# Kernel optimization log

Measured on AMD Instinct MI355X. Metric: run time of the kernel, lower is better.

The kernel has to match this reference:

```python
import jax, jax.numpy as jnp
import numpy as np

NUM_FEATURES = 8
HIDDEN = 64
IN_DIM = NUM_FEATURES + 6  # 14


def _lstm_cell(x, h, c, W_ih, W_hh, b_ih, b_hh):
    # torch gate order: i, f, g, o
    gates = x @ W_ih.T + h @ W_hh.T + b_ih + b_hh
    i, f, g, o = jnp.split(gates, 4, axis=-1)
    c_new = jax.nn.sigmoid(f) * c + jax.nn.sigmoid(i) * jnp.tanh(g)
    h_new = jax.nn.sigmoid(o) * jnp.tanh(c_new)
    return h_new, c_new


def setup_inputs() -> dict:
    key = jax.random.key(0)
    ks = jax.random.split(key, 20)
    T = 20000
    s = 0.05
    inp = {
        "encoder_out": jax.random.normal(ks[0], (1024, 64), jnp.float32),
        "h0": jax.random.normal(ks[1], (2, HIDDEN), jnp.float32),
        "c0": jax.random.normal(ks[2], (2, HIDDEN), jnp.float32),
        "difficulty": jax.random.normal(ks[3], (6,), jnp.float32),
        "target": jax.random.normal(ks[4], (T, NUM_FEATURES), jnp.float32),
        # LSTM layer 0 (input 14 -> hidden 64)
        "W_ih0": jax.random.normal(ks[5], (4 * HIDDEN, IN_DIM), jnp.float32) * s,
        "W_hh0": jax.random.normal(ks[6], (4 * HIDDEN, HIDDEN), jnp.float32) * s,
        "b_ih0": jax.random.normal(ks[7], (4 * HIDDEN,), jnp.float32) * s,
        "b_hh0": jax.random.normal(ks[8], (4 * HIDDEN,), jnp.float32) * s,
        # LSTM layer 1 (hidden 64 -> hidden 64)
        "W_ih1": jax.random.normal(ks[9], (4 * HIDDEN, HIDDEN), jnp.float32) * s,
        "W_hh1": jax.random.normal(ks[10], (4 * HIDDEN, HIDDEN), jnp.float32) * s,
        "b_ih1": jax.random.normal(ks[11], (4 * HIDDEN,), jnp.float32) * s,
        "b_hh1": jax.random.normal(ks[12], (4 * HIDDEN,), jnp.float32) * s,
        # hiddenfc: 64 -> 32
        "W_hid": jax.random.normal(ks[13], (HIDDEN // 2, HIDDEN), jnp.float32) * s,
        "b_hid": jax.random.normal(ks[14], (HIDDEN // 2,), jnp.float32) * s,
        # outputfc: 32 -> 8
        "W_out": jax.random.normal(ks[15], (NUM_FEATURES, HIDDEN // 2), jnp.float32) * s,
        "b_out": jax.random.normal(ks[16], (NUM_FEATURES,), jnp.float32) * s,
    }
    return inp


def reference(encoder_out, h0, c0, difficulty, target,
              W_ih0, W_hh0, b_ih0, b_hh0,
              W_ih1, W_hh1, b_ih1, b_hh1,
              W_hid, b_hid, W_out, b_out):
    T = target.shape[0]
    # Teacher-forced inputs: step 0 is zeros(14); step i>0 is cat(target[i-1], difficulty).
    diff_tiled = jnp.broadcast_to(difficulty, (T - 1, 6))
    inputs = jnp.concatenate([
        jnp.zeros((1, IN_DIM), target.dtype),
        jnp.concatenate([target[:-1], diff_tiled], axis=1),
    ], axis=0)  # [T, 14]

    def step(carry, x_t):
        h0s, c0s, h1s, c1s = carry
        h0s, c0s = _lstm_cell(x_t, h0s, c0s, W_ih0, W_hh0, b_ih0, b_hh0)
        h1s, c1s = _lstm_cell(h0s, h1s, c1s, W_ih1, W_hh1, b_ih1, b_hh1)
        # dropout is identity in eval mode
        hid = h1s @ W_hid.T + b_hid
        out = jnp.round(hid @ W_out.T + b_out)
        return (h0s, c0s, h1s, c1s), out

    init = (h0[0], c0[0], h0[1], c0[1])
    (hf0, cf0, hf1, cf1), outs = jax.lax.scan(step, init, inputs)
    h_final = jnp.stack([hf0, hf1])  # [2, 64]
    c_final = jnp.stack([cf0, cf1])  # [2, 64]
    return outs, h_final, c_final
```

## Files before the change

kernel.cpp:

```cpp
#include <hip/hip_runtime.h>

#define NF 8
#define RD 256
#define RMASK 255

typedef float f2 __attribute__((ext_vector_type(2)));
typedef float f4 __attribute__((ext_vector_type(4)));

template <int CTRL>
__device__ __forceinline__ float qp(float x) {
  return __int_as_float(
      __builtin_amdgcn_update_dpp(0, __float_as_int(x), CTRL, 0xF, 0xF, true));
}

__device__ __forceinline__ void wg_barrier() {
  asm volatile("s_waitcnt lgkmcnt(0)" ::: "memory");
  __builtin_amdgcn_s_barrier();
  __builtin_amdgcn_sched_barrier(0);
}

#define WAIT_VM(N) asm volatile("s_waitcnt vmcnt(" #N ")" ::: "memory")

__device__ __forceinline__ float ld_cohf(const float* p) {
  float v;
  asm volatile("global_load_dword %0, %1, off sc0 sc1" : "=v"(v) : "v"(p) : "memory");
  return v;
}
__device__ __forceinline__ int ld_cohi(const int* p) {
  int v;
  asm volatile("global_load_dword %0, %1, off sc0 sc1" : "=v"(v) : "v"(p) : "memory");
  return v;
}
__device__ __forceinline__ void st_cohf(float* p, float v) {
  asm volatile("global_store_dword %0, %1, off sc0 sc1" :: "v"(p), "v"(v) : "memory");
}
__device__ __forceinline__ void st_cohi(int* p, int v) {
  asm volatile("global_store_dword %0, %1, off sc0 sc1" :: "v"(p), "v"(v) : "memory");
}

__global__ __launch_bounds__(320, 1) void decoder_p14(
    const float* __restrict__ h0in, const float* __restrict__ c0in,
    const float* __restrict__ diffp, const float* __restrict__ target,
    const float* __restrict__ Wih0, const float* __restrict__ Whh0,
    const float* __restrict__ bih0, const float* __restrict__ bhh0,
    const float* __restrict__ Wih1, const float* __restrict__ Whh1,
    const float* __restrict__ bih1, const float* __restrict__ bhh1,
    const float* __restrict__ Whid, const float* __restrict__ bhidp,
    const float* __restrict__ Woutp, const float* __restrict__ boutp,
    float* __restrict__ outp, float* __restrict__ ws, const int T)
{
  const int tid = threadIdx.x;
  const int wv  = tid >> 6;
  const int l   = tid & 63;
  const int q   = l >> 2;
  const int k   = l & 3;
  const int u   = 16 * (wv & 3) + q;
  const int r   = 64 * k + u;
  const bool isk0 = (k == 0);
  const float am = (k == 2) ? 2.0f : 1.0f;
  const float ab = (k == 2) ? -1.0f : 0.0f;

  __shared__ alignas(256) float h0r[4][64];
  __shared__ alignas(256) float tbuf[2][32 * NF];
  __shared__ alignas(256) float h0loc[16][64];
  __shared__ alignas(256) float h1r[4][64];
  __shared__ alignas(256) float h1loc[8][64];
  __shared__ alignas(256) float hidS[4][32];
  __shared__ float ldspad[20480];

  if (T < 0) {
    ldspad[tid] = h0in[tid];
    __syncthreads();
    outp[0] = ldspad[319 - tid];
  }

  int* flag0p = (int*)ws;
  int* cons0p = (int*)ws + 16;
  int* flag1p = (int*)ws + 32;
  int* cons1p = (int*)ws + 48;
  float* ring0 = ws + 256;
  float* ring1 = ws + 256 + RD * 64;

  if (blockIdx.x == 0) {
    f2 wreg[36];
    float b_ = 0.f, xd = 0.f, cS = 0.f, hS = 0.f, xc = 0.f;
    if (wv < 4) {
      #pragma unroll
      for (int j = 0; j < 4; ++j) {
        const int row = 64 * ((k + j) & 3) + u;
        const float* rp = Whh0 + row * 64 + 16 * k;
        #pragma unroll
        for (int c = 0; c < 4; ++c) {
          f4 v = *(const f4*)(rp + 4 * ((c + k) & 3));
          wreg[8 * j + 2 * c]     = v.lo;
          wreg[8 * j + 2 * c + 1] = v.hi;
        }
      }
      b_ = bih0[r] + bhh0[r];
      const float* ra = Wih0 + r * 14;
      #pragma unroll
      for (int c = 0; c < 4; ++c) wreg[32 + c] = (f2){ra[2 * c], ra[2 * c + 1]};
      #pragma unroll
      for (int m = 0; m < 6; ++m) xd += ra[8 + m] * diffp[m];
      if (isk0) cS = c0in[u];
      if (wv == 0) h0r[3][l] = h0in[l];
    } else {
      if (l < T) {
        *(f4*)&((float*)tbuf)[l * 8]     = *(const f4*)&target[l * 8];
        *(f4*)&((float*)tbuf)[l * 8 + 4] = *(const f4*)&target[l * 8 + 4];
      }
    }
    __syncthreads();
    if (wv < 4) __builtin_amdgcn_s_setprio(1);

    int cons0L = 0;
    f4 tr0 = {0.f, 0.f, 0.f, 0.f}, tr1 = {0.f, 0.f, 0.f, 0.f};
    for (int t = 0; t <= T; ++t) {
      if (wv < 4) {
        if (t < T) {
          const float* base = &h0r[(t - 1) & 3][16 * k];
          f2 P0 = {0.f,0.f}, P1 = {0.f,0.f}, P2 = {0.f,0.f}, P3 = {0.f,0.f};
          #pragma unroll
          for (int c = 0; c < 4; ++c) {
            f4 v = *(const f4*)(base + 4 * ((c + k) & 3));
            P0 += wreg[2*c] * v.lo;      P0 += wreg[2*c+1] * v.hi;
            P1 += wreg[8+2*c] * v.lo;    P1 += wreg[8+2*c+1] * v.hi;
            P2 += wreg[16+2*c] * v.lo;   P2 += wreg[16+2*c+1] * v.hi;
            P3 += wreg[24+2*c] * v.lo;   P3 += wreg[24+2*c+1] * v.hi;
          }
          float p0 = P0.x + P0.y, p1 = P1.x + P1.y;
          float p2 = P2.x + P2.y, p3 = P3.x + P3.y;
          float g = ((p0 + qp<0x39>(p3)) + (qp<0x4E>(p2) + qp<0x93>(p1))) + b_ + xc;
          float e = __expf(-g * am);
          float s = __fdividef(1.0f, 1.0f + e);
          float a = fmaf(s, am, ab);
          float A1 = qp<0xB1>(a), A2 = qp<0x4E>(a), A3 = qp<0x1B>(a);
          if (isk0) {
            cS = A1 * cS + a * A2;
            float e2 = __expf(-2.0f * cS);
            hS = A3 * (__fdividef(2.0f, 1.0f + e2) - 1.0f);
            h0r[t & 3][u] = hS;
          }
        }
        if (t < T - 1) {
          const f4* trow = (const f4*)&tbuf[(t >> 5) & 1][(t & 31) * NF];
          f4 r0 = trow[0], r1 = trow[1];
          f2 s2 = wreg[32] * r0.lo; s2 += wreg[33] * r0.hi;
          s2 += wreg[34] * r1.lo;   s2 += wreg[35] * r1.hi;
          xc = xd + s2.x + s2.y;
        } else xc = 0.f;
      } else {
        if ((t & 3) == 0 && t >= 8) {
          WAIT_VM(4);
          if (l == 0) st_cohi(flag0p, t - 6);
        }
        if ((t & 63) == 0 && t > RD - 64) {
          while (t - cons0L > RD - 64) {
            cons0L = ld_cohi(cons0p);
            WAIT_VM(0);
          }
        }
        if (t >= 1) {
          float hv = h0r[(t - 1) & 3][l];
          st_cohf(&ring0[((t - 1) & RMASK) * 64 + l], hv);
        }
        const int ph = t & 31;
        const int cl = (t >> 5) + 1;
        if (l < 32 && cl * 32 < T) {
          if (ph == 8) {
            tr0 = *(const f4*)&target[cl * 256 + l * 8];
            tr1 = *(const f4*)&target[cl * 256 + l * 8 + 4];
          } else if (ph == 26) {
            *(f4*)&tbuf[cl & 1][l * 8]     = tr0;
            *(f4*)&tbuf[cl & 1][l * 8 + 4] = tr1;
          }
        }
      }
      wg_barrier();
    }
    if (wv == 4) {
      WAIT_VM(0);
      if (l == 0) st_cohi(flag0p, T);
    }
    if (wv < 4 && isk0) {
      outp[T * NF + u]       = hS;
      outp[T * NF + 128 + u] = cS;
    }
  } else if (blockIdx.x == 1) {
    f2 wreg[64];
    float b_ = 0.f, cS = 0.f, hS = 0.f;
    if (wv < 4) {
      const float* Wsrc = (k < 2) ? Wih1 : Whh1;
      const int co = 32 * (k & 1);
      #pragma unroll
      for (int j = 0; j < 4; ++j) {
        const int row = 64 * ((k + j) & 3) + u;
        const float* rp = Wsrc + row * 64 + co;
        #pragma unroll
        for (int c = 0; c < 8; ++c) {
          f4 v = *(const f4*)(rp + 4 * ((c + 2 * k) & 7));
          wreg[16 * j + 2 * c]     = v.lo;
          wreg[16 * j + 2 * c + 1] = v.hi;
        }
      }
      b_ = bih1[r] + bhh1[r];
      if (isk0) cS = c0in[64 + u];
      if (wv == 0) h1r[3][l] = h0in[64 + l];
    }
    int flagL = 0, fillW = 0, nPend = 0, F_pend = 0, cons1L = 0;
    float pb0 = 0.f, pb1 = 0.f, pb2 = 0.f, pb3 = 0.f;
    if (wv == 4) {
      const int pre = (T < 4) ? T : 4;
      while (flagL < pre) {
        flagL = ld_cohi(flag0p);
        WAIT_VM(0);
      }
      for (int s = 0; s < pre; ++s) {
        float v = ld_cohf(&ring0[(s & RMASK) * 64 + l]);
        WAIT_VM(0);
        h0loc[s & 15][l] = v;
      }
      fillW = pre;
      F_pend = flagL;
    }
    __syncthreads();
    if (wv < 4) __builtin_amdgcn_s_setprio(1);

    for (int p = 0; p <= T; ++p) {
      if (wv < 4) {
        if (p < T) {
          const float* base = (k < 2) ? &h0loc[p & 15][32 * (k & 1)]
                                      : &h1r[(p - 1) & 3][32 * (k & 1)];
          f2 P0 = {0.f,0.f}, P1 = {0.f,0.f}, P2 = {0.f,0.f}, P3 = {0.f,0.f};
          #pragma unroll
          for (int c = 0; c < 8; ++c) {
            f4 v = *(const f4*)(base + 4 * ((c + 2 * k) & 7));
            P0 += wreg[2*c] * v.lo;      P0 += wreg[2*c+1] * v.hi;
            P1 += wreg[16+2*c] * v.lo;   P1 += wreg[16+2*c+1] * v.hi;
            P2 += wreg[32+2*c] * v.lo;   P2 += wreg[32+2*c+1] * v.hi;
            P3 += wreg[48+2*c] * v.lo;   P3 += wreg[48+2*c+1] * v.hi;
          }
          float p0 = P0.x + P0.y, p1 = P1.x + P1.y;
          float p2 = P2.x + P2.y, p3 = P3.x + P3.y;
          float g = ((p0 + qp<0x39>(p3)) + (qp<0x4E>(p2) + qp<0x93>(p1))) + b_;
          float e = __expf(-g * am);
          float s = __fdividef(1.0f, 1.0f + e);
          float a = fmaf(s, am, ab);
          float A1 = qp<0xB1>(a), A2 = qp<0x4E>(a), A3 = qp<0x1B>(a);
          if (isk0) {
            cS = A1 * cS + a * A2;
            float e2 = __expf(-2.0f * cS);
            hS = A3 * (__fdividef(2.0f, 1.0f + e2) - 1.0f);
            h1r[p & 3][u] = hS;
          }
        }
      } else if (wv == 4) {
        WAIT_VM(1);
        if (nPend > 0) h0loc[(fillW + 0) & 15][l] = pb0;
        if (nPend > 1) h0loc[(fillW + 1) & 15][l] = pb1;
        if (nPend > 2) h0loc[(fillW + 2) & 15][l] = pb2;
        if (nPend > 3) h0loc[(fillW + 3) & 15][l] = pb3;
        fillW += nPend;
        nPend = 0;
        if ((p & 3) == 1) flagL = F_pend;
        {
          int need = p + 2; if (need > T) need = T;
          while (fillW < need) {
            while (flagL < fillW + 1) {
              flagL = ld_cohi(flag0p);
              WAIT_VM(0);
            }
            float v = ld_cohf(&ring0[(fillW & RMASK) * 64 + l]);
            WAIT_VM(0);
            h0loc[fillW & 15][l] = v;
            ++fillW;
          }
        }
        if ((p & 3) == 0 && p >= 8 && l == 0)
          st_cohi(flag1p, p - 6);
        if ((p & 63) == 0 && p > RD - 64) {
          while (p - cons1L > RD - 64) {
            cons1L = ld_cohi(cons1p);
            WAIT_VM(0);
          }
        }
        if ((p & 3) == 0) F_pend = ld_cohi(flag0p);
        {
          int want = flagL;
          if (want > p + 10) want = p + 10;
          if (want > T) want = T;
          int n = want - fillW;
          if (n < 0) n = 0;
          if (n > 4) n = 4;
          if (n > 0) pb0 = ld_cohf(&ring0[((fillW + 0) & RMASK) * 64 + l]);
          if (n > 1) pb1 = ld_cohf(&ring0[((fillW + 1) & RMASK) * 64 + l]);
          if (n > 2) pb2 = ld_cohf(&ring0[((fillW + 2) & RMASK) * 64 + l]);
          if (n > 3) pb3 = ld_cohf(&ring0[((fillW + 3) & RMASK) * 64 + l]);
          nPend = n;
        }
        if (p >= 1) {
          float hv = h1r[(p - 1) & 3][l];
          st_cohf(&ring1[((p - 1) & RMASK) * 64 + l], hv);
        }
        if ((p & 63) == 32 && l == 0) st_cohi(cons0p, fillW);
      }
      wg_barrier();
    }
    if (wv == 4) {
      WAIT_VM(0);
      if (l == 0) st_cohi(flag1p, T);
    }
    if (wv < 4 && isk0) {
      outp[T * NF + 64 + u]  = hS;
      outp[T * NF + 192 + u] = cS;
    }
  } else {
    if (wv != 0) return;
    f2 wH[16], wO[4];
    float bhA = 0.f, bhB = 0.f, bo_ = 0.f;
    #pragma unroll
    for (int i = 0; i < 2; ++i) {
      const float* rp = Whid + (2 * q + i) * 64 + 16 * k;
      #pragma unroll
      for (int c = 0; c < 4; ++c) {
        f4 v = *(const f4*)(rp + 4 * ((c + k) & 3));
        wH[8 * i + 2 * c]     = v.lo;
        wH[8 * i + 2 * c + 1] = v.hi;
      }
    }
    bhA = bhidp[2 * q];
    bhB = bhidp[2 * q + 1];
    if (q < 8) {
      const float* rp = Woutp + q * 32 + 8 * k;
      #pragma unroll
      for (int c = 0; c < 2; ++c) {
        f4 v = *(const f4*)(rp + 4 * ((c + k) & 1));
        wO[2 * c]     = v.lo;
        wO[2 * c + 1] = v.hi;
      }
      bo_ = boutp[q];
    }
    int f1L = 0;
    for (int s0 = 0; s0 < T; s0 += 8) {
      const int B = (T - s0 < 8) ? (T - s0) : 8;
      while (f1L < s0 + B) {
        f1L = ld_cohi(flag1p);
        WAIT_VM(0);
      }
      float rb[8];
      #pragma unroll
      for (int i = 0; i < 8; ++i)
        if (i < B) rb[i] = ld_cohf(&ring1[((s0 + i) & RMASK) * 64 + l]);
      WAIT_VM(0);
      #pragma unroll
      for (int i = 0; i < 8; ++i)
        if (i < B) h1loc[(s0 + i) & 7][l] = rb[i];
      #pragma unroll
      for (int i = 0; i < 8; ++i) {
        if (i < B) {
          const int s = s0 + i;
          const float* hp = &h1loc[s & 7][16 * k];
          f2 pa = {0.f,0.f}, pb = {0.f,0.f};
          #pragma unroll
          for (int c = 0; c < 4; ++c) {
            f4 v = *(const f4*)(hp + 4 * ((c + k) & 3));
            pa += wH[2*c] * v.lo;     pa += wH[2*c+1] * v.hi;
            pb += wH[8+2*c] * v.lo;   pb += wH[8+2*c+1] * v.hi;
          }
          float sa = pa.x + pa.y; sa += qp<0xB1>(sa); sa += qp<0x4E>(sa);
          float sb = pb.x + pb.y; sb += qp<0xB1>(sb); sb += qp<0x4E>(sb);
          if (isk0) *(f2*)&hidS[s & 3][2 * q] = (f2){sa + bhA, sb + bhB};
          if (q < 8) {
            const float* hq = &hidS[s & 3][8 * k];
            f2 po = {0.f,0.f};
            #pragma unroll
            for (int c = 0; c < 2; ++c) {
              f4 v = *(const f4*)(hq + 4 * ((c + k) & 1));
              po += wO[2*c] * v.lo; po += wO[2*c+1] * v.hi;
            }
            float so = po.x + po.y; so += qp<0xB1>(so); so += qp<0x4E>(so);
            if (isk0) outp[s * NF + q] = rintf(so + bo_);
          }
        }
      }
      if ((s0 & 63) == 0 && s0 > 0 && l == 0) st_cohi(cons1p, s0);
    }
  }
}

extern "C" void kernel_launch(void* const* d_in, const int* in_sizes, int n_in,
                              void* d_out, int out_size, void* d_ws, size_t ws_size,
                              hipStream_t stream) {
  const float* h0in   = (const float*)d_in[1];
  const float* c0in   = (const float*)d_in[2];
  const float* diffp  = (const float*)d_in[3];
  const float* target = (const float*)d_in[4];
  const float* Wih0   = (const float*)d_in[5];
  const float* Whh0   = (const float*)d_in[6];
  const float* bih0   = (const float*)d_in[7];
  const float* bhh0   = (const float*)d_in[8];
  const float* Wih1   = (const float*)d_in[9];
  const float* Whh1   = (const float*)d_in[10];
  const float* bih1   = (const float*)d_in[11];
  const float* bhh1   = (const float*)d_in[12];
  const float* Whid   = (const float*)d_in[13];
  const float* bhidp  = (const float*)d_in[14];
  const float* Woutp  = (const float*)d_in[15];
  const float* boutp  = (const float*)d_in[16];
  float* outp = (float*)d_out;
  const int T = in_sizes[4] / NF;

  hipMemsetAsync(d_ws, 0, 256, stream);
  decoder_p14<<<dim3(3), dim3(320), 0, stream>>>(
      h0in, c0in, diffp, target,
      Wih0, Whh0, bih0, bhh0,
      Wih1, Whh1, bih1, bhh1,
      Whid, bhidp, Woutp, boutp,
      outp, (float*)d_ws, T);
}
```

Measured before the change: 10.51 ms.

## Fuse output head into layer-1 block and pipeline global ring polling

Drops the third block that read layer-1 hidden states through a global ring. Its hidden/output FC work moves into a sixth wave of the layer-1 block, which computes it from shared memory two and four steps behind and buffers the outputs in LDS for periodic coalesced stores. The producer/consumer handshake on ring0 now issues flag and consumer-counter loads every step into rotating register slots, so polls overlap instead of blocking. The loader wave also prefetches deeper. This removes the second cross-block ring and its latency, at the cost of more complex bookkeeping and a wider block.

```diff
diff --git a/kernel.cpp b/kernel.cpp
--- a/kernel.cpp
+++ b/kernel.cpp
@@ -38,7 +38,7 @@
   asm volatile("global_store_dword %0, %1, off sc0 sc1" :: "v"(p), "v"(v) : "memory");
 }
 
-__global__ __launch_bounds__(320, 1) void decoder_p14(
+__global__ __launch_bounds__(384, 1) void decoder_p15(
     const float* __restrict__ h0in, const float* __restrict__ c0in,
     const float* __restrict__ diffp, const float* __restrict__ target,
     const float* __restrict__ Wih0, const float* __restrict__ Whh0,
@@ -64,22 +64,19 @@
   __shared__ alignas(256) float tbuf[2][32 * NF];
   __shared__ alignas(256) float h0loc[16][64];
   __shared__ alignas(256) float h1r[4][64];
-  __shared__ alignas(256) float h1loc[8][64];
   __shared__ alignas(256) float hidS[4][32];
+  __shared__ alignas(256) float obuf[64 * NF];
   __shared__ float ldspad[20480];
 
   if (T < 0) {
     ldspad[tid] = h0in[tid];
     __syncthreads();
-    outp[0] = ldspad[319 - tid];
+    outp[0] = ldspad[383 - tid];
   }
 
   int* flag0p = (int*)ws;
   int* cons0p = (int*)ws + 16;
-  int* flag1p = (int*)ws + 32;
-  int* cons1p = (int*)ws + 48;
   float* ring0 = ws + 256;
-  float* ring1 = ws + 256 + RD * 64;
 
   if (blockIdx.x == 0) {
     f2 wreg[36];
@@ -104,7 +101,7 @@
       for (int m = 0; m < 6; ++m) xd += ra[8 + m] * diffp[m];
       if (isk0) cS = c0in[u];
       if (wv == 0) h0r[3][l] = h0in[l];
-    } else {
+    } else if (wv == 5) {
       if (l < T) {
         *(f4*)&((float*)tbuf)[l * 8]     = *(const f4*)&target[l * 8];
         *(f4*)&((float*)tbuf)[l * 8 + 4] = *(const f4*)&target[l * 8 + 4];
@@ -113,8 +110,12 @@
     __syncthreads();
     if (wv < 4) __builtin_amdgcn_s_setprio(1);
 
+    int cpol[8];
+    #pragma unroll
+    for (int ii = 0; ii < 8; ++ii) cpol[ii] = 0;
     int cons0L = 0;
     f4 tr0 = {0.f, 0.f, 0.f, 0.f}, tr1 = {0.f, 0.f, 0.f, 0.f};
+
     for (int t = 0; t <= T; ++t) {
       if (wv < 4) {
         if (t < T) {
@@ -149,12 +150,15 @@
           s2 += wreg[34] * r1.lo;   s2 += wreg[35] * r1.hi;
           xc = xd + s2.x + s2.y;
         } else xc = 0.f;
-      } else {
-        if ((t & 3) == 0 && t >= 8) {
-          WAIT_VM(4);
-          if (l == 0) st_cohi(flag0p, t - 6);
-        }
-        if ((t & 63) == 0 && t > RD - 64) {
+      } else if (wv == 4) {
+        if (t < 16) { WAIT_VM(0); } else { WAIT_VM(20); }
+        const int i8 = t & 7;
+        #pragma unroll
+        for (int ii = 0; ii < 8; ++ii) if (ii == i8) {
+          if (cpol[ii] > cons0L) cons0L = cpol[ii];
+        }
+        if (t - cons0L > RD - 64) {
+          WAIT_VM(0);
           while (t - cons0L > RD - 64) {
             cons0L = ld_cohi(cons0p);
             WAIT_VM(0);
@@ -164,6 +168,14 @@
           float hv = h0r[(t - 1) & 3][l];
           st_cohf(&ring0[((t - 1) & RMASK) * 64 + l], hv);
         }
+        {
+          int fv = t - 7; if (fv < 0) fv = 0;
+          if (l == 0) st_cohi(flag0p, fv);
+        }
+        #pragma unroll
+        for (int ii = 0; ii < 8; ++ii) if (ii == i8)
+          cpol[ii] = ld_cohi(cons0p);
+      } else {
         const int ph = t & 31;
         const int cl = (t >> 5) + 1;
         if (l < 32 && cl * 32 < T) {
@@ -171,6 +183,7 @@
             tr0 = *(const f4*)&target[cl * 256 + l * 8];
             tr1 = *(const f4*)&target[cl * 256 + l * 8 + 4];
           } else if (ph == 26) {
+            WAIT_VM(0);
             *(f4*)&tbuf[cl & 1][l * 8]     = tr0;
             *(f4*)&tbuf[cl & 1][l * 8 + 4] = tr1;
           }
@@ -186,9 +199,11 @@
       outp[T * NF + u]       = hS;
       outp[T * NF + 128 + u] = cS;
     }
-  } else if (blockIdx.x == 1) {
+  } else {
     f2 wreg[64];
+    f2 wH[16], wO[4];
     float b_ = 0.f, cS = 0.f, hS = 0.f;
+    float bhA = 0.f, bhB = 0.f, bo_ = 0.f;
     if (wv < 4) {
       const float* Wsrc = (k < 2) ? Wih1 : Whh1;
       const int co = 32 * (k & 1);
@@ -206,27 +221,54 @@
       b_ = bih1[r] + bhh1[r];
       if (isk0) cS = c0in[64 + u];
       if (wv == 0) h1r[3][l] = h0in[64 + l];
-    }
-    int flagL = 0, fillW = 0, nPend = 0, F_pend = 0, cons1L = 0;
-    float pb0 = 0.f, pb1 = 0.f, pb2 = 0.f, pb3 = 0.f;
+    } else if (wv == 5) {
+      #pragma unroll
+      for (int i = 0; i < 2; ++i) {
+        const float* rp = Whid + (2 * q + i) * 64 + 16 * k;
+        #pragma unroll
+        for (int c = 0; c < 4; ++c) {
+          f4 v = *(const f4*)(rp + 4 * ((c + k) & 3));
+          wH[8 * i + 2 * c]     = v.lo;
+          wH[8 * i + 2 * c + 1] = v.hi;
+        }
+      }
+      bhA = bhidp[2 * q];
+      bhB = bhidp[2 * q + 1];
+      if (q < 8) {
+        const float* rp = Woutp + q * 32 + 8 * k;
+        #pragma unroll
+        for (int c = 0; c < 2; ++c) {
+          f4 v = *(const f4*)(rp + 4 * ((c + k) & 1));
+          wO[2 * c]     = v.lo;
+          wO[2 * c + 1] = v.hi;
+        }
+        bo_ = boutp[q];
+      }
+    }
+    float pend[8];
+    int ps[8], fpol[8];
+    #pragma unroll
+    for (int ii = 0; ii < 8; ++ii) { pend[ii] = 0.f; ps[ii] = -1; fpol[ii] = 0; }
+    int flagL = 0, fillW = 0, fillPub = 0;
     if (wv == 4) {
-      const int pre = (T < 4) ? T : 4;
-      while (flagL < pre) {
+      const int pf = (T < 16) ? T : 16;
+      while (flagL < pf) {
         flagL = ld_cohi(flag0p);
         WAIT_VM(0);
       }
-      for (int s = 0; s < pre; ++s) {
+      for (int s = 0; s < pf; ++s) {
         float v = ld_cohf(&ring0[(s & RMASK) * 64 + l]);
         WAIT_VM(0);
         h0loc[s & 15][l] = v;
       }
-      fillW = pre;
-      F_pend = flagL;
+      fillW = pf;
+      fillPub = pf;
     }
     __syncthreads();
     if (wv < 4) __builtin_amdgcn_s_setprio(1);
 
-    for (int p = 0; p <= T; ++p) {
+    const int pend_ = T + 4;
+    for (int p = 0; p <= pend_; ++p) {
       if (wv < 4) {
         if (p < T) {
           const float* base = (k < 2) ? &h0loc[p & 15][32 * (k & 1)]
@@ -255,111 +297,66 @@
           }
         }
       } else if (wv == 4) {
-        WAIT_VM(1);
-        if (nPend > 0) h0loc[(fillW + 0) & 15][l] = pb0;
-        if (nPend > 1) h0loc[(fillW + 1) & 15][l] = pb1;
-        if (nPend > 2) h0loc[(fillW + 2) & 15][l] = pb2;
-        if (nPend > 3) h0loc[(fillW + 3) & 15][l] = pb3;
-        fillW += nPend;
-        nPend = 0;
-        if ((p & 3) == 1) flagL = F_pend;
-        {
-          int need = p + 2; if (need > T) need = T;
-          while (fillW < need) {
-            while (flagL < fillW + 1) {
+        if (p < 8) { WAIT_VM(0); } else { WAIT_VM(20); }
+        const int i8 = p & 7;
+        const int wr = (i8 + 1) & 7;
+        #pragma unroll
+        for (int ii = 0; ii < 8; ++ii) if (ii == wr) {
+          if (ps[ii] >= 0) {
+            h0loc[ps[ii] & 15][l] = pend[ii];
+            if (ps[ii] + 1 > fillPub) fillPub = ps[ii] + 1;
+            ps[ii] = -1;
+          }
+        }
+        #pragma unroll
+        for (int ii = 0; ii < 8; ++ii) if (ii == i8) {
+          if (fpol[ii] > flagL) flagL = fpol[ii];
+        }
+        if (fillPub < p + 2 && fillPub < T) {
+          WAIT_VM(0);
+          #pragma unroll
+          for (int ii = 0; ii < 8; ++ii) {
+            if (ps[ii] >= 0) {
+              h0loc[ps[ii] & 15][l] = pend[ii];
+              if (ps[ii] + 1 > fillPub) fillPub = ps[ii] + 1;
+              ps[ii] = -1;
+            }
+          }
+          if (fillW < fillPub) fillW = fillPub;
+          int need = p + 8; if (need > T) need = T;
+          while (fillPub < need) {
+            while (flagL < fillPub + 1) {
               flagL = ld_cohi(flag0p);
               WAIT_VM(0);
             }
-            float v = ld_cohf(&ring0[(fillW & RMASK) * 64 + l]);
+            float v = ld_cohf(&ring0[(fillPub & RMASK) * 64 + l]);
             WAIT_VM(0);
-            h0loc[fillW & 15][l] = v;
-            ++fillW;
-          }
-        }
-        if ((p & 3) == 0 && p >= 8 && l == 0)
-          st_cohi(flag1p, p - 6);
-        if ((p & 63) == 0 && p > RD - 64) {
-          while (p - cons1L > RD - 64) {
-            cons1L = ld_cohi(cons1p);
-            WAIT_VM(0);
-          }
-        }
-        if ((p & 3) == 0) F_pend = ld_cohi(flag0p);
+            h0loc[fillPub & 15][l] = v;
+            ++fillPub;
+          }
+          if (fillW < fillPub) fillW = fillPub;
+        }
         {
-          int want = flagL;
-          if (want > p + 10) want = p + 10;
-          if (want > T) want = T;
-          int n = want - fillW;
-          if (n < 0) n = 0;
-          if (n > 4) n = 4;
-          if (n > 0) pb0 = ld_cohf(&ring0[((fillW + 0) & RMASK) * 64 + l]);
-          if (n > 1) pb1 = ld_cohf(&ring0[((fillW + 1) & RMASK) * 64 + l]);
-          if (n > 2) pb2 = ld_cohf(&ring0[((fillW + 2) & RMASK) * 64 + l]);
-          if (n > 3) pb3 = ld_cohf(&ring0[((fillW + 3) & RMASK) * 64 + l]);
-          nPend = n;
-        }
-        if (p >= 1) {
-          float hv = h1r[(p - 1) & 3][l];
-          st_cohf(&ring1[((p - 1) & RMASK) * 64 + l], hv);
-        }
-        if ((p & 63) == 32 && l == 0) st_cohi(cons0p, fillW);
-      }
-      wg_barrier();
-    }
-    if (wv == 4) {
-      WAIT_VM(0);
-      if (l == 0) st_cohi(flag1p, T);
-    }
-    if (wv < 4 && isk0) {
-      outp[T * NF + 64 + u]  = hS;
-      outp[T * NF + 192 + u] = cS;
-    }
-  } else {
-    if (wv != 0) return;
-    f2 wH[16], wO[4];
-    float bhA = 0.f, bhB = 0.f, bo_ = 0.f;
-    #pragma unroll
-    for (int i = 0; i < 2; ++i) {
-      const float* rp = Whid + (2 * q + i) * 64 + 16 * k;
-      #pragma unroll
-      for (int c = 0; c < 4; ++c) {
-        f4 v = *(const f4*)(rp + 4 * ((c + k) & 3));
-        wH[8 * i + 2 * c]     = v.lo;
-        wH[8 * i + 2 * c + 1] = v.hi;
-      }
-    }
-    bhA = bhidp[2 * q];
-    bhB = bhidp[2 * q + 1];
-    if (q < 8) {
-      const float* rp = Woutp + q * 32 + 8 * k;
-      #pragma unroll
-      for (int c = 0; c < 2; ++c) {
-        f4 v = *(const f4*)(rp + 4 * ((c + k) & 1));
-        wO[2 * c]     = v.lo;
-        wO[2 * c + 1] = v.hi;
-      }
-      bo_ = boutp[q];
-    }
-    int f1L = 0;
-    for (int s0 = 0; s0 < T; s0 += 8) {
-      const int B = (T - s0 < 8) ? (T - s0) : 8;
-      while (f1L < s0 + B) {
-        f1L = ld_cohi(flag1p);
-        WAIT_VM(0);
-      }
-      float rb[8];
-      #pragma unroll
-      for (int i = 0; i < 8; ++i)
-        if (i < B) rb[i] = ld_cohf(&ring1[((s0 + i) & RMASK) * 64 + l]);
-      WAIT_VM(0);
-      #pragma unroll
-      for (int i = 0; i < 8; ++i)
-        if (i < B) h1loc[(s0 + i) & 7][l] = rb[i];
-      #pragma unroll
-      for (int i = 0; i < 8; ++i) {
-        if (i < B) {
-          const int s = s0 + i;
-          const float* hp = &h1loc[s & 7][16 * k];
+          int cap = p + 20;
+          if (cap > flagL) cap = flagL;
+          if (cap > T) cap = T;
+          const bool ok = (fillW < cap);
+          const float* ap = ok ? &ring0[(fillW & RMASK) * 64 + l] : &ring0[l];
+          #pragma unroll
+          for (int ii = 0; ii < 8; ++ii) if (ii == i8) {
+            pend[ii] = ld_cohf(ap);
+            ps[ii] = ok ? fillW : -1;
+          }
+          if (ok) ++fillW;
+        }
+        #pragma unroll
+        for (int ii = 0; ii < 8; ++ii) if (ii == i8)
+          fpol[ii] = ld_cohi(flag0p);
+        if (l == 0) st_cohi(cons0p, fillPub);
+      } else {
+        const int sH = p - 2;
+        if (sH >= 0 && sH < T) {
+          const float* hp = &h1r[sH & 3][16 * k];
           f2 pa = {0.f,0.f}, pb = {0.f,0.f};
           #pragma unroll
           for (int c = 0; c < 4; ++c) {
@@ -369,21 +366,45 @@
           }
           float sa = pa.x + pa.y; sa += qp<0xB1>(sa); sa += qp<0x4E>(sa);
           float sb = pb.x + pb.y; sb += qp<0xB1>(sb); sb += qp<0x4E>(sb);
-          if (isk0) *(f2*)&hidS[s & 3][2 * q] = (f2){sa + bhA, sb + bhB};
-          if (q < 8) {
-            const float* hq = &hidS[s & 3][8 * k];
-            f2 po = {0.f,0.f};
-            #pragma unroll
-            for (int c = 0; c < 2; ++c) {
-              f4 v = *(const f4*)(hq + 4 * ((c + k) & 1));
-              po += wO[2*c] * v.lo; po += wO[2*c+1] * v.hi;
-            }
-            float so = po.x + po.y; so += qp<0xB1>(so); so += qp<0x4E>(so);
-            if (isk0) outp[s * NF + q] = rintf(so + bo_);
-          }
-        }
-      }
-      if ((s0 & 63) == 0 && s0 > 0 && l == 0) st_cohi(cons1p, s0);
+          if (isk0) *(f2*)&hidS[sH & 3][2 * q] = (f2){sa + bhA, sb + bhB};
+        }
+        const int sO = p - 4;
+        if (sO >= 0 && sO < T && q < 8) {
+          const float* hp = &hidS[sO & 3][8 * k];
+          f2 po = {0.f,0.f};
+          #pragma unroll
+          for (int c = 0; c < 2; ++c) {
+            f4 v = *(const f4*)(hp + 4 * ((c + k) & 1));
+            po += wO[2*c] * v.lo; po += wO[2*c+1] * v.hi;
+          }
+          float so = po.x + po.y; so += qp<0xB1>(so); so += qp<0x4E>(so);
+          if (isk0) obuf[(sO & 63) * NF + q] = rintf(so + bo_);
+        }
+        if (l >= 32 && (p & 31) == 5 && p >= 37) {
+          const int j = l - 32;
+          #pragma unroll
+          for (int ii = 0; ii < 2; ++ii) {
+            const int fidx = 2 * j + ii;
+            const int s  = (p - 37) + (fidx >> 1);
+            const int c4 = (fidx & 1) * 4;
+            *(f4*)&outp[s * NF + c4] = *(const f4*)&obuf[(s & 63) * NF + c4];
+          }
+        }
+      }
+      wg_barrier();
+    }
+    if (wv < 4 && isk0) {
+      outp[T * NF + 64 + u]  = hS;
+      outp[T * NF + 192 + u] = cS;
+    }
+    __syncthreads();
+    {
+      int s0 = T - 64;
+      if (s0 < 0) s0 = 0;
+      for (int idx = tid; idx < (T - s0) * NF; idx += 384) {
+        const int s = s0 + (idx >> 3);
+        outp[s * NF + (idx & 7)] = obuf[(s & 63) * NF + (idx & 7)];
+      }
     }
   }
 }
@@ -411,7 +432,7 @@
   const int T = in_sizes[4] / NF;
 
   hipMemsetAsync(d_ws, 0, 256, stream);
-  decoder_p14<<<dim3(3), dim3(320), 0, stream>>>(
+  decoder_p15<<<dim3(2), dim3(384), 0, stream>>>(
       h0in, c0in, diffp, target,
       Wih0, Whh0, bih0, bhh0,
       Wih1, Whh1, bih1, bhh1,
```

Result: slower. 15.25 ms (+45.1%).

## Use sentinel-filled full-length ring to drop flag sync and fuse output block

Applied to the files above, without the earlier changes.

When the workspace is large enough, the host pre-fills a full-length h0 buffer with a sentinel pattern. Layer 1 then polls the data itself for non-sentinel values instead of waiting on flag and consumer counters, which removes the flag round trips between blocks. The separate third block for the output head is folded into an extra wave of the layer-1 block. That wave reads h1 from LDS with a pipelined lag and writes outputs through an LDS staging buffer in coalesced chunks, so the ring1 handoff through global memory disappears. The cost is a memset over T*64 floats before each launch, plus a sentinel test that would misfire if a real value equalled the sentinel bit pattern (a NaN).

```diff
diff --git a/kernel.cpp b/kernel.cpp
--- a/kernel.cpp
+++ b/kernel.cpp
@@ -1,8 +1,8 @@
 #include <hip/hip_runtime.h>
 
 #define NF 8
-#define RD 256
 #define RMASK 255
+#define SENT 0xFFFFFFFFu
 
 typedef float f2 __attribute__((ext_vector_type(2)));
 typedef float f4 __attribute__((ext_vector_type(4)));
@@ -38,7 +38,7 @@
   asm volatile("global_store_dword %0, %1, off sc0 sc1" :: "v"(p), "v"(v) : "memory");
 }
 
-__global__ __launch_bounds__(320, 1) void decoder_p14(
+__global__ __launch_bounds__(384, 1) void decoder_p18(
     const float* __restrict__ h0in, const float* __restrict__ c0in,
     const float* __restrict__ diffp, const float* __restrict__ target,
     const float* __restrict__ Wih0, const float* __restrict__ Whh0,
@@ -47,7 +47,8 @@
     const float* __restrict__ bih1, const float* __restrict__ bhh1,
     const float* __restrict__ Whid, const float* __restrict__ bhidp,
     const float* __restrict__ Woutp, const float* __restrict__ boutp,
-    float* __restrict__ outp, float* __restrict__ ws, const int T)
+    float* __restrict__ outp, float* __restrict__ ws, const int T,
+    const int BP)
 {
   const int tid = threadIdx.x;
   const int wv  = tid >> 6;
@@ -64,22 +65,19 @@
   __shared__ alignas(256) float tbuf[2][32 * NF];
   __shared__ alignas(256) float h0loc[16][64];
   __shared__ alignas(256) float h1r[4][64];
-  __shared__ alignas(256) float h1loc[8][64];
   __shared__ alignas(256) float hidS[4][32];
+  __shared__ alignas(256) float obuf[64 * NF];
   __shared__ float ldspad[20480];
 
   if (T < 0) {
     ldspad[tid] = h0in[tid];
     __syncthreads();
-    outp[0] = ldspad[319 - tid];
+    outp[0] = ldspad[383 - tid];
   }
 
   int* flag0p = (int*)ws;
-  int* cons0p = (int*)ws + 16;
-  int* flag1p = (int*)ws + 32;
-  int* cons1p = (int*)ws + 48;
+  int* cons0p = (int*)ws + 64;
   float* ring0 = ws + 256;
-  float* ring1 = ws + 256 + RD * 64;
 
   if (blockIdx.x == 0) {
     f2 wreg[36];
@@ -104,7 +102,7 @@
       for (int m = 0; m < 6; ++m) xd += ra[8 + m] * diffp[m];
       if (isk0) cS = c0in[u];
       if (wv == 0) h0r[3][l] = h0in[l];
-    } else {
+    } else if (wv == 5) {
       if (l < T) {
         *(f4*)&((float*)tbuf)[l * 8]     = *(const f4*)&target[l * 8];
         *(f4*)&((float*)tbuf)[l * 8 + 4] = *(const f4*)&target[l * 8 + 4];
@@ -149,21 +147,29 @@
           s2 += wreg[34] * r1.lo;   s2 += wreg[35] * r1.hi;
           xc = xd + s2.x + s2.y;
         } else xc = 0.f;
+      } else if (wv == 4) {
+        if (!BP) {
+          if (t >= 1) {
+            float hv = h0r[(t - 1) & 3][l];
+            st_cohf(&ring0[(t - 1) * 64 + l], hv);
+          }
+        } else {
+          if ((t & 3) == 0 && t >= 8) {
+            WAIT_VM(4);
+            if (l == 0) st_cohi(flag0p, t - 6);
+          }
+          if ((t & 63) == 0 && t > 192) {
+            while (t - cons0L > 192) {
+              cons0L = ld_cohi(cons0p);
+              WAIT_VM(0);
+            }
+          }
+          if (t >= 1) {
+            float hv = h0r[(t - 1) & 3][l];
+            st_cohf(&ring0[((t - 1) & RMASK) * 64 + l], hv);
+          }
+        }
       } else {
-        if ((t & 3) == 0 && t >= 8) {
-          WAIT_VM(4);
-          if (l == 0) st_cohi(flag0p, t - 6);
-        }
-        if ((t & 63) == 0 && t > RD - 64) {
-          while (t - cons0L > RD - 64) {
-            cons0L = ld_cohi(cons0p);
-            WAIT_VM(0);
-          }
-        }
-        if (t >= 1) {
-          float hv = h0r[(t - 1) & 3][l];
-          st_cohf(&ring0[((t - 1) & RMASK) * 64 + l], hv);
-        }
         const int ph = t & 31;
         const int cl = (t >> 5) + 1;
         if (l < 32 && cl * 32 < T) {
@@ -171,6 +177,7 @@
             tr0 = *(const f4*)&target[cl * 256 + l * 8];
             tr1 = *(const f4*)&target[cl * 256 + l * 8 + 4];
           } else if (ph == 26) {
+            WAIT_VM(0);
             *(f4*)&tbuf[cl & 1][l * 8]     = tr0;
             *(f4*)&tbuf[cl & 1][l * 8 + 4] = tr1;
           }
@@ -178,7 +185,7 @@
       }
       wg_barrier();
     }
-    if (wv == 4) {
+    if (BP && wv == 4) {
       WAIT_VM(0);
       if (l == 0) st_cohi(flag0p, T);
     }
@@ -186,9 +193,11 @@
       outp[T * NF + u]       = hS;
       outp[T * NF + 128 + u] = cS;
     }
-  } else if (blockIdx.x == 1) {
+  } else {
     f2 wreg[64];
+    f2 wH[16], wO[4];
     float b_ = 0.f, cS = 0.f, hS = 0.f;
+    float bhA = 0.f, bhB = 0.f, bo_ = 0.f;
     if (wv < 4) {
       const float* Wsrc = (k < 2) ? Wih1 : Whh1;
       const int co = 32 * (k & 1);
@@ -206,27 +215,65 @@
       b_ = bih1[r] + bhh1[r];
       if (isk0) cS = c0in[64 + u];
       if (wv == 0) h1r[3][l] = h0in[64 + l];
-    }
-    int flagL = 0, fillW = 0, nPend = 0, F_pend = 0, cons1L = 0;
+    } else if (wv == 5) {
+      #pragma unroll
+      for (int i = 0; i < 2; ++i) {
+        const float* rp = Whid + (2 * q + i) * 64 + 16 * k;
+        #pragma unroll
+        for (int c = 0; c < 4; ++c) {
+          f4 v = *(const f4*)(rp + 4 * ((c + k) & 3));
+          wH[8 * i + 2 * c]     = v.lo;
+          wH[8 * i + 2 * c + 1] = v.hi;
+        }
+      }
+      bhA = bhidp[2 * q];
+      bhB = bhidp[2 * q + 1];
+      if (q < 8) {
+        const float* rp = Woutp + q * 32 + 8 * k;
+        #pragma unroll
+        for (int c = 0; c < 2; ++c) {
+          f4 v = *(const f4*)(rp + 4 * ((c + k) & 1));
+          wO[2 * c]     = v.lo;
+          wO[2 * c + 1] = v.hi;
+        }
+        bo_ = boutp[q];
+      }
+    }
+    __syncthreads();
+
     float pb0 = 0.f, pb1 = 0.f, pb2 = 0.f, pb3 = 0.f;
+    int ns = 0, fillW = 0, flagL = 0, F_pend = 0, nPend = 0;
     if (wv == 4) {
-      const int pre = (T < 4) ? T : 4;
-      while (flagL < pre) {
-        flagL = ld_cohi(flag0p);
-        WAIT_VM(0);
-      }
-      for (int s = 0; s < pre; ++s) {
-        float v = ld_cohf(&ring0[(s & RMASK) * 64 + l]);
-        WAIT_VM(0);
-        h0loc[s & 15][l] = v;
-      }
-      fillW = pre;
-      F_pend = flagL;
+      if (!BP) {
+        const int pf = (T < 8) ? T : 8;
+        while (fillW < pf) {
+          float v = ld_cohf(&ring0[fillW * 64 + l]);
+          WAIT_VM(0);
+          if (__all(__float_as_uint(v) != SENT)) {
+            h0loc[fillW & 15][l] = v;
+            ++fillW;
+          }
+        }
+      } else {
+        const int pf = (T < 4) ? T : 4;
+        while (flagL < pf) {
+          flagL = ld_cohi(flag0p);
+          WAIT_VM(0);
+        }
+        for (int s = 0; s < pf; ++s) {
+          float v = ld_cohf(&ring0[(s & RMASK) * 64 + l]);
+          WAIT_VM(0);
+          h0loc[s & 15][l] = v;
+        }
+        fillW = pf;
+        F_pend = flagL;
+      }
     }
     __syncthreads();
     if (wv < 4) __builtin_amdgcn_s_setprio(1);
 
-    for (int p = 0; p <= T; ++p) {
+    const int pend_ = T + 4;
+    for (int p = 0; p <= pend_; ++p) {
       if (wv < 4) {
         if (p < T) {
           const float* base = (k < 2) ? &h0loc[p & 15][32 * (k & 1)]
@@ -255,111 +302,88 @@
           }
         }
       } else if (wv == 4) {
-        WAIT_VM(1);
-        if (nPend > 0) h0loc[(fillW + 0) & 15][l] = pb0;
-        if (nPend > 1) h0loc[(fillW + 1) & 15][l] = pb1;
-        if (nPend > 2) h0loc[(fillW + 2) & 15][l] = pb2;
-        if (nPend > 3) h0loc[(fillW + 3) & 15][l] = pb3;
-        fillW += nPend;
-        nPend = 0;
-        if ((p & 3) == 1) flagL = F_pend;
-        {
-          int need = p + 2; if (need > T) need = T;
-          while (fillW < need) {
-            while (flagL < fillW + 1) {
-              flagL = ld_cohi(flag0p);
+        if (!BP) {
+          WAIT_VM(0);
+          bool stop = false;
+          if (ns > 0 && !stop) {
+            if (__all(__float_as_uint(pb0) != SENT)) { h0loc[fillW & 15][l] = pb0; ++fillW; }
+            else stop = true;
+          }
+          if (ns > 1 && !stop) {
+            if (__all(__float_as_uint(pb1) != SENT)) { h0loc[fillW & 15][l] = pb1; ++fillW; }
+            else stop = true;
+          }
+          if (ns > 2 && !stop) {
+            if (__all(__float_as_uint(pb2) != SENT)) { h0loc[fillW & 15][l] = pb2; ++fillW; }
+            else stop = true;
+          }
+          if (ns > 3 && !stop) {
+            if (__all(__float_as_uint(pb3) != SENT)) { h0loc[fillW & 15][l] = pb3; ++fillW; }
+            else stop = true;
+          }
+          ns = 0;
+          {
+            int lim = p + 2; if (lim > T) lim = T;
+            while (fillW < lim) {
+              float v = ld_cohf(&ring0[fillW * 64 + l]);
               WAIT_VM(0);
+              if (__all(__float_as_uint(v) != SENT)) {
+                h0loc[fillW & 15][l] = v;
+                ++fillW;
+              }
             }
-            float v = ld_cohf(&ring0[(fillW & RMASK) * 64 + l]);
-            WAIT_VM(0);
-            h0loc[fillW & 15][l] = v;
-            ++fillW;
-          }
-        }
-        if ((p & 3) == 0 && p >= 8 && l == 0)
-          st_cohi(flag1p, p - 6);
-        if ((p & 63) == 0 && p > RD - 64) {
-          while (p - cons1L > RD - 64) {
-            cons1L = ld_cohi(cons1p);
-            WAIT_VM(0);
-          }
-        }
-        if ((p & 3) == 0) F_pend = ld_cohi(flag0p);
-        {
-          int want = flagL;
-          if (want > p + 10) want = p + 10;
-          if (want > T) want = T;
-          int n = want - fillW;
-          if (n < 0) n = 0;
-          if (n > 4) n = 4;
-          if (n > 0) pb0 = ld_cohf(&ring0[((fillW + 0) & RMASK) * 64 + l]);
-          if (n > 1) pb1 = ld_cohf(&ring0[((fillW + 1) & RMASK) * 64 + l]);
-          if (n > 2) pb2 = ld_cohf(&ring0[((fillW + 2) & RMASK) * 64 + l]);
-          if (n > 3) pb3 = ld_cohf(&ring0[((fillW + 3) & RMASK) * 64 + l]);
-          nPend = n;
-        }
-        if (p >= 1) {
-          float hv = h1r[(p - 1) & 3][l];
-          st_cohf(&ring1[((p - 1) & RMASK) * 64 + l], hv);
-        }
-        if ((p & 63) == 32 && l == 0) st_cohi(cons0p, fillW);
-      }
-      wg_barrier();
-    }
-    if (wv == 4) {
-      WAIT_VM(0);
-      if (l == 0) st_cohi(flag1p, T);
-    }
-    if (wv < 4 && isk0) {
-      outp[T * NF + 64 + u]  = hS;
-      outp[T * NF + 192 + u] = cS;
-    }
-  } else {
-    if (wv != 0) return;
-    f2 wH[16], wO[4];
-    float bhA = 0.f, bhB = 0.f, bo_ = 0.f;
-    #pragma unroll
-    for (int i = 0; i < 2; ++i) {
-      const float* rp = Whid + (2 * q + i) * 64 + 16 * k;
-      #pragma unroll
-      for (int c = 0; c < 4; ++c) {
-        f4 v = *(const f4*)(rp + 4 * ((c + k) & 3));
-        wH[8 * i + 2 * c]     = v.lo;
-        wH[8 * i + 2 * c + 1] = v.hi;
-      }
-    }
-    bhA = bhidp[2 * q];
-    bhB = bhidp[2 * q + 1];
-    if (q < 8) {
-      const float* rp = Woutp + q * 32 + 8 * k;
-      #pragma unroll
-      for (int c = 0; c < 2; ++c) {
-        f4 v = *(const f4*)(rp + 4 * ((c + k) & 1));
-        wO[2 * c]     = v.lo;
-        wO[2 * c + 1] = v.hi;
-      }
-      bo_ = boutp[q];
-    }
-    int f1L = 0;
-    for (int s0 = 0; s0 < T; s0 += 8) {
-      const int B = (T - s0 < 8) ? (T - s0) : 8;
-      while (f1L < s0 + B) {
-        f1L = ld_cohi(flag1p);
-        WAIT_VM(0);
-      }
-      float rb[8];
-      #pragma unroll
-      for (int i = 0; i < 8; ++i)
-        if (i < B) rb[i] = ld_cohf(&ring1[((s0 + i) & RMASK) * 64 + l]);
-      WAIT_VM(0);
-      #pragma unroll
-      for (int i = 0; i < 8; ++i)
-        if (i < B) h1loc[(s0 + i) & 7][l] = rb[i];
-      #pragma unroll
-      for (int i = 0; i < 8; ++i) {
-        if (i < B) {
-          const int s = s0 + i;
-          const float* hp = &h1loc[s & 7][16 * k];
+          }
+          {
+            int want = p + 14; if (want > T) want = T;
+            int n = want - fillW; if (n < 0) n = 0; if (n > 4) n = 4;
+            if (n > 0) pb0 = ld_cohf(&ring0[(fillW + 0) * 64 + l]);
+            if (n > 1) pb1 = ld_cohf(&ring0[(fillW + 1) * 64 + l]);
+            if (n > 2) pb2 = ld_cohf(&ring0[(fillW + 2) * 64 + l]);
+            if (n > 3) pb3 = ld_cohf(&ring0[(fillW + 3) * 64 + l]);
+            ns = n;
+          }
+        } else {
+          WAIT_VM(0);
+          if (nPend > 0) h0loc[(fillW + 0) & 15][l] = pb0;
+          if (nPend > 1) h0loc[(fillW + 1) & 15][l] = pb1;
+          if (nPend > 2) h0loc[(fillW + 2) & 15][l] = pb2;
+          if (nPend > 3) h0loc[(fillW + 3) & 15][l] = pb3;
+          fillW += nPend;
+          nPend = 0;
+          if ((p & 3) == 1) flagL = F_pend;
+          {
+            int need = p + 2; if (need > T) need = T;
+            while (fillW < need) {
+              while (flagL < fillW + 1) {
+                flagL = ld_cohi(flag0p);
+                WAIT_VM(0);
+              }
+              float v = ld_cohf(&ring0[(fillW & RMASK) * 64 + l]);
+              WAIT_VM(0);
+              h0loc[fillW & 15][l] = v;
+              ++fillW;
+            }
+          }
+          if ((p & 3) == 0) F_pend = ld_cohi(flag0p);
+          {
+            int want = flagL;
+            if (want > p + 10) want = p + 10;
+            if (want > T) want = T;
+            int n = want - fillW;
+            if (n < 0) n = 0;
+            if (n > 4) n = 4;
+            if (n > 0) pb0 = ld_cohf(&ring0[((fillW + 0) & RMASK) * 64 + l]);
+            if (n > 1) pb1 = ld_cohf(&ring0[((fillW + 1) & RMASK) * 64 + l]);
+            if (n > 2) pb2 = ld_cohf(&ring0[((fillW + 2) & RMASK) * 64 + l]);
+            if (n > 3) pb3 = ld_cohf(&ring0[((fillW + 3) & RMASK) * 64 + l]);
+            nPend = n;
+          }
+          if ((p & 63) == 32 && l == 0) st_cohi(cons0p, fillW);
+        }
+      } else {
+        const int sH = p - 2;
+        if (sH >= 0 && sH < T) {
+          const float* hp = &h1r[sH & 3][16 * k];
           f2 pa = {0.f,0.f}, pb = {0.f,0.f};
           #pragma unroll
           for (int c = 0; c < 4; ++c) {
@@ -369,21 +393,45 @@
           }
           float sa = pa.x + pa.y; sa += qp<0xB1>(sa); sa += qp<0x4E>(sa);
           float sb = pb.x + pb.y; sb += qp<0xB1>(sb); sb += qp<0x4E>(sb);
-          if (isk0) *(f2*)&hidS[s & 3][2 * q] = (f2){sa + bhA, sb + bhB};
-          if (q < 8) {
-            const float* hq = &hidS[s & 3][8 * k];
-            f2 po = {0.f,0.f};
-            #pragma unroll
-            for (int c = 0; c < 2; ++c) {
-              f4 v = *(const f4*)(hq + 4 * ((c + k) & 1));
-              po += wO[2*c] * v.lo; po += wO[2*c+1] * v.hi;
-            }
-            float so = po.x + po.y; so += qp<0xB1>(so); so += qp<0x4E>(so);
-            if (isk0) outp[s * NF + q] = rintf(so + bo_);
-          }
-        }
-      }
-      if ((s0 & 63) == 0 && s0 > 0 && l == 0) st_cohi(cons1p, s0);
+          if (isk0) *(f2*)&hidS[sH & 3][2 * q] = (f2){sa + bhA, sb + bhB};
+        }
+        const int sO = p - 4;
+        if (sO >= 0 && sO < T && q < 8) {
+          const float* hp = &hidS[sO & 3][8 * k];
+          f2 po = {0.f,0.f};
+          #pragma unroll
+          for (int c = 0; c < 2; ++c) {
+            f4 v = *(const f4*)(hp + 4 * ((c + k) & 1));
+            po += wO[2*c] * v.lo; po += wO[2*c+1] * v.hi;
+          }
+          float so = po.x + po.y; so += qp<0xB1>(so); so += qp<0x4E>(so);
+          if (isk0) obuf[(sO & 63) * NF + q] = rintf(so + bo_);
+        }
+        if (l >= 32 && (p & 31) == 5 && p >= 37) {
+          const int j = l - 32;
+          #pragma unroll
+          for (int ii = 0; ii < 2; ++ii) {
+            const int fidx = 2 * j + ii;
+            const int s  = (p - 37) + (fidx >> 1);
+            const int c4 = (fidx & 1) * 4;
+            *(f4*)&outp[s * NF + c4] = *(const f4*)&obuf[(s & 63) * NF + c4];
+          }
+        }
+      }
+      wg_barrier();
+    }
+    if (wv < 4 && isk0) {
+      outp[T * NF + 64 + u]  = hS;
+      outp[T * NF + 192 + u] = cS;
+    }
+    __syncthreads();
+    {
+      int s0 = T - 64;
+      if (s0 < 0) s0 = 0;
+      for (int idx = tid; idx < (T - s0) * NF; idx += 384) {
+        const int s = s0 + (idx >> 3);
+        outp[s * NF + (idx & 7)] = obuf[(s & 63) * NF + (idx & 7)];
+      }
     }
   }
 }
@@ -410,11 +458,20 @@
   float* outp = (float*)d_out;
   const int T = in_sizes[4] / NF;
 
-  hipMemsetAsync(d_ws, 0, 256, stream);
-  decoder_p14<<<dim3(3), dim3(320), 0, stream>>>(
+  const size_t need = ((size_t)256 + (size_t)T * 64) * 4;
+  int BP;
+  if (ws_size >= need) {
+    BP = 0;
+    hipMemsetAsync(d_ws, 0xFF, need, stream);
+  } else {
+    BP = 1;
+    hipMemsetAsync(d_ws, 0, 1024, stream);
+  }
+
+  decoder_p18<<<dim3(2), dim3(384), 0, stream>>>(
       h0in, c0in, diffp, target,
       Wih0, Whh0, bih0, bhh0,
       Wih1, Whh1, bih1, bhh1,
       Whid, bhidp, Woutp, boutp,
-      outp, (float*)d_ws, T);
-}
+      outp, (float*)d_ws, T, BP);
+}
```

Measured after the change: 9.878 ms. 6.0% less time.
